# Performance work log

Measured on AMD Instinct MI355X. Metric: run time of the kernel, lower is better.

The kernel has to match this reference:

```python
import jax, jax.numpy as jnp
import numpy as np

N = 100_000   # nodes
E = 800_000   # edges
F_IN = 128    # num_features
E_IN = 64     # edge_dim
H = 100       # n_hidden
L = 2         # num_gnn_layers
BN_EPS = 1e-5


def _lin(key, fan_in, fan_out, extra=()):
    kw, _ = jax.random.split(key)
    w = jax.random.normal(kw, (*extra, fan_in, fan_out), jnp.float32) / np.float32(np.sqrt(fan_in))
    b = jnp.zeros((*extra, fan_out), jnp.float32)
    return w, b


def setup_inputs() -> dict:
    key = jax.random.key(0)
    ks = jax.random.split(key, 12)
    x = jax.random.normal(ks[0], (N, F_IN), jnp.float32)
    edge_index = jax.random.randint(ks[1], (2, E), 0, N, dtype=jnp.int32)
    edge_attr = jax.random.normal(ks[2], (E, E_IN), jnp.float32)
    node_w, node_b = _lin(ks[3], F_IN, H)
    edge_w, edge_b = _lin(ks[4], E_IN, H)
    lin_w, lin_b = _lin(ks[5], H, H, (L,))   # GINEConv edge lin per layer
    w1, b1 = _lin(ks[6], H, H, (L,))         # GINEConv nn first Linear
    w2, b2 = _lin(ks[7], H, H, (L,))         # GINEConv nn second Linear
    gamma = jnp.ones((L, H), jnp.float32)
    beta = jnp.zeros((L, H), jnp.float32)
    ew1, eb1 = _lin(ks[8], 3 * H, H, (L,))   # edge-update MLP
    ew2, eb2 = _lin(ks[9], H, H, (L,))
    mw1, mb1 = _lin(ks[10], 3 * H, 50)
    k11, k12 = jax.random.split(ks[11])
    mw2, mb2 = _lin(k11, 50, 25)
    mw3, mb3 = _lin(k12, 25, 2)
    return dict(x=x, edge_index=edge_index, edge_attr=edge_attr,
                node_w=node_w, node_b=node_b, edge_w=edge_w, edge_b=edge_b,
                lin_w=lin_w, lin_b=lin_b, w1=w1, b1=b1, w2=w2, b2=b2,
                gamma=gamma, beta=beta, ew1=ew1, eb1=eb1, ew2=ew2, eb2=eb2,
                mw1=mw1, mb1=mb1, mw2=mw2, mb2=mb2, mw3=mw3, mb3=mb3)


def reference(x, edge_index, edge_attr, node_w, node_b, edge_w, edge_b,
              lin_w, lin_b, w1, b1, w2, b2, gamma, beta,
              ew1, eb1, ew2, eb2, mw1, mb1, mw2, mb2, mw3, mb3):
    src, dst = edge_index[0], edge_index[1]
    h = x @ node_w + node_b          # [N, H]
    e = edge_attr @ edge_w + edge_b  # [E, H]
    for i in range(L):
        # GINEConv: message = relu(x_src + lin(edge_attr)); sum-aggregate at dst
        msg = jax.nn.relu(h[src] + (e @ lin_w[i] + lin_b[i]))       # [E, H]
        agg = jax.ops.segment_sum(msg, dst, num_segments=N)         # [N, H]
        z = h + agg                                                  # (1+eps)*x + aggr, eps=0
        z = jax.nn.relu(z @ w1[i] + b1[i]) @ w2[i] + b2[i]
        # BatchNorm over nodes (training mode, biased variance)
        mu = z.mean(0)
        var = z.var(0)
        z = (z - mu) * jax.lax.rsqrt(var + BN_EPS) * gamma[i] + beta[i]
        h = (h + jax.nn.relu(z)) / 2
        # edge update: emlp(cat(x_src, x_dst, e))
        cat = jnp.concatenate([h[src], h[dst], e], axis=-1)         # [E, 3H]
        e = e + (jax.nn.relu(cat @ ew1[i] + eb1[i]) @ ew2[i] + eb2[i]) / 2
    feat = jnp.concatenate(
        [jax.nn.relu(jnp.concatenate([h[src], h[dst]], axis=-1)), e], axis=1)  # [E, 3H]
    out = jax.nn.relu(feat @ mw1 + mb1)
    out = jax.nn.relu(out @ mw2 + mb2)
    return out @ mw3 + mb3  # [E, 2]
```

## Files before the change

### kernel.cpp

```cpp
#include <hip/hip_runtime.h>

#define N_NODES 100000
#define N_EDGES 800000
#define HDIM 100
#define LDP 112
#define TSTR 104

typedef __attribute__((ext_vector_type(8))) short bf16x8;
typedef __attribute__((ext_vector_type(4))) float f32x4;

__device__ inline uint packsplit(float v) {
    uint u = __float_as_uint(v);
    float r = v - __uint_as_float(u & 0xFFFF0000u);
    return (u & 0xFFFF0000u) | (__float_as_uint(r) >> 16);
}
__device__ inline float recw(uint w) {
    return __uint_as_float(w & 0xFFFF0000u) + __uint_as_float(w << 16);
}
__device__ inline uint4 relu4(uint4 a) {
    a.x &= ~(uint)((int)a.x >> 31); a.y &= ~(uint)((int)a.y >> 31);
    a.z &= ~(uint)((int)a.z >> 31); a.w &= ~(uint)((int)a.w >> 31);
    return a;
}
__device__ inline void unpack16(uint4 a, uint4 b, bf16x8& h8, bf16x8& l8) {
    union { uint u[4]; bf16x8 v; } H, L;
    H.u[0] = __builtin_amdgcn_perm(a.y, a.x, 0x07060302u);
    H.u[1] = __builtin_amdgcn_perm(a.w, a.z, 0x07060302u);
    H.u[2] = __builtin_amdgcn_perm(b.y, b.x, 0x07060302u);
    H.u[3] = __builtin_amdgcn_perm(b.w, b.z, 0x07060302u);
    L.u[0] = __builtin_amdgcn_perm(a.y, a.x, 0x05040100u);
    L.u[1] = __builtin_amdgcn_perm(a.w, a.z, 0x05040100u);
    L.u[2] = __builtin_amdgcn_perm(b.y, b.x, 0x05040100u);
    L.u[3] = __builtin_amdgcn_perm(b.w, b.z, 0x05040100u);
    h8 = H.v; l8 = L.v;
}
__device__ inline void split8(float4 a, float4 b, bf16x8& h8, bf16x8& l8) {
    float v[8] = {a.x, a.y, a.z, a.w, b.x, b.y, b.z, b.w};
    bf16x8 hh, ll;
#pragma unroll
    for (int i = 0; i < 8; ++i) {
        uint u = __float_as_uint(v[i]);
        hh[i] = (short)(u >> 16);
        float r = v[i] - __uint_as_float(u & 0xFFFF0000u);
        ll[i] = (short)(__float_as_uint(r) >> 16);
    }
    h8 = hh; l8 = ll;
}

template<int CONCAT>
__global__ __launch_bounds__(256)
void pack_k(const float* __restrict__ W, ushort* __restrict__ hi, ushort* __restrict__ lo,
            int K, int NC, int Kpad, int NCpad, int total)
{
    int idx = blockIdx.x * 256 + threadIdx.x;
    if (idx >= total) return;
    int per = NCpad * Kpad;
    int b = idx / per, rem = idx - b * per;
    int col = rem / Kpad, kv = rem - col * Kpad;
    int srck; bool valid;
    if (CONCAT) {
        int seg = kv >> 7, off = kv & 127;
        srck = seg * 100 + off;
        valid = (off < 100) && (srck < K) && (col < NC);
    } else {
        srck = kv;
        valid = (kv < K) && (col < NC);
    }
    float v = valid ? W[(long)b * K * NC + (long)srck * NC + col] : 0.f;
    uint w = packsplit(v);
    hi[idx] = (ushort)(w >> 16);
    lo[idx] = (ushort)(w & 0xFFFFu);
}

template<int TILES, int TPW, int STEPS, int MODE, int GATHER, int AFP32, int OUTF32, int CLAMP>
__global__ __launch_bounds__(256, 2)
void gemm9_k(const uint* aP, int lda, const float* __restrict__ aF, int ldaf,
             const ushort* __restrict__ wH, const ushort* __restrict__ wL,
             const float* __restrict__ bias,
             float* __restrict__ Cf, uint* cP, int ldc,
             int M, int NC, const int* __restrict__ g0)
{
    constexpr int KPADW = STEPS * 32;
    const int tid  = threadIdx.x;
    const int lane = tid & 63;
    const int w    = tid >> 6;
    const int cl   = lane & 15;
    const int kgrp = lane >> 4;
    const long row0 = (long)blockIdx.x * 64;

    int arows[4];
#pragma unroll
    for (int rg = 0; rg < 4; ++rg) {
        long grow = row0 + rg * 16 + cl;
        int gc = (int)((grow < M) ? grow : (M - 1));
        arows[rg] = (GATHER == 3) ? g0[gc] : gc;
    }

    uint4  aw0[2][4], aw1[2][4];
    float4 af0[2][4], af1[2][4];
    bf16x8 bh[2][TPW], bl[2][TPW];
    f32x4  acc[TPW][4];
#pragma unroll
    for (int tp = 0; tp < TPW; ++tp)
#pragma unroll
        for (int rg = 0; rg < 4; ++rg) acc[tp][rg] = (f32x4){0.f, 0.f, 0.f, 0.f};

    auto loadA = [&](int st, int sl) {
        const int kk = st * 32 + kgrp * 8;
#pragma unroll
        for (int rg = 0; rg < 4; ++rg) {
            if (AFP32) {
                const float* p = aF + (size_t)arows[rg] * ldaf + kk;
                af0[sl][rg] = *(const float4*)p;
                af1[sl][rg] = *(const float4*)(p + 4);
            } else {
                bool ok = !CLAMP || ((st & 3) != 3) || (kgrp == 0);
                if (ok) {
                    const uint* p = aP + (size_t)arows[rg] * lda + kk;
                    aw0[sl][rg] = *(const uint4*)p;
                    aw1[sl][rg] = *(const uint4*)(p + 4);
                } else {
                    aw0[sl][rg] = make_uint4(0, 0, 0, 0);
                    aw1[sl][rg] = make_uint4(0, 0, 0, 0);
                }
            }
        }
    };
    auto loadB = [&](int st, int sl) {
        int kk = st * 32 + kgrp * 8;
#pragma unroll
        for (int tp = 0; tp < TPW; ++tp) {
            int colw = (w * TPW + tp) * 16 + cl;
            bh[sl][tp] = *(const bf16x8*)(wH + (size_t)colw * KPADW + kk);
            bl[sl][tp] = *(const bf16x8*)(wL + (size_t)colw * KPADW + kk);
        }
    };

    loadA(0, 0); loadB(0, 0);
    if (STEPS > 1) { loadA(1, 1); loadB(1, 1); }

#pragma unroll
    for (int st = 0; st < STEPS; ++st) {
        const int sl = st & 1;
#pragma unroll
        for (int rg = 0; rg < 4; ++rg) {
            bf16x8 aH, aL;
            if (AFP32) split8(af0[sl][rg], af1[sl][rg], aH, aL);
            else       unpack16(aw0[sl][rg], aw1[sl][rg], aH, aL);
#pragma unroll
            for (int tp = 0; tp < TPW; ++tp) {
                acc[tp][rg] = __builtin_amdgcn_mfma_f32_16x16x32_bf16(aL, bh[sl][tp], acc[tp][rg], 0, 0, 0);
                acc[tp][rg] = __builtin_amdgcn_mfma_f32_16x16x32_bf16(aH, bl[sl][tp], acc[tp][rg], 0, 0, 0);
                acc[tp][rg] = __builtin_amdgcn_mfma_f32_16x16x32_bf16(aH, bh[sl][tp], acc[tp][rg], 0, 0, 0);
            }
        }
        if (st + 2 < STEPS) { loadA(st + 2, sl); loadB(st + 2, sl); }
    }

#pragma unroll
    for (int tp = 0; tp < TPW; ++tp) {
        int col = (w * TPW + tp) * 16 + cl;
        if (col >= NC) continue;
        float bv = bias[col];
#pragma unroll
        for (int rg = 0; rg < 4; ++rg) {
#pragma unroll
            for (int i = 0; i < 4; ++i) {
                long grow = row0 + rg * 16 + kgrp * 4 + i;
                if (grow >= M) continue;
                float v = acc[tp][rg][i] + bv;
                if (MODE == 1) v = fmaxf(v, 0.f);
                long o = grow * (long)ldc + col;
                if (OUTF32) Cf[o] = v;
                else        cP[o] = packsplit(v);
            }
        }
    }
}

__global__ __launch_bounds__(256, 2)
void fused_edge_k(const uint* __restrict__ hP, uint* eP,
                  const ushort* __restrict__ w1H, const ushort* __restrict__ w1L,
                  const float* __restrict__ b1v,
                  const ushort* __restrict__ w2H, const ushort* __restrict__ w2L,
                  const float* __restrict__ b2v,
                  const int* __restrict__ g0, const int* __restrict__ g1)
{
    __shared__ uint sm[64 * 128];
    const int tid = threadIdx.x, lane = tid & 63, w = tid >> 6;
    const int cl = lane & 15, kgrp = lane >> 4;
    const long row0 = (long)blockIdx.x * 64;

    int rs[4], rd[4];
#pragma unroll
    for (int rg = 0; rg < 4; ++rg) {
        long gr = row0 + rg * 16 + cl;
        rs[rg] = g0[gr]; rd[rg] = g1[gr];
    }

    uint4 aw0[2][4], aw1[2][4];
    bf16x8 bh[2][2], bl[2][2];
    f32x4 acc[2][4];
#pragma unroll
    for (int tp = 0; tp < 2; ++tp)
#pragma unroll
        for (int rg = 0; rg < 4; ++rg) acc[tp][rg] = (f32x4){0.f, 0.f, 0.f, 0.f};

    auto loadA = [&](int st, int sl) {
        int seg = st >> 2, inseg = (st & 3) * 32 + kgrp * 8;
        bool ok = ((st & 3) != 3) || (kgrp == 0);
        const uint* base = (seg == 2) ? eP : hP;
#pragma unroll
        for (int rg = 0; rg < 4; ++rg) {
            if (ok) {
                long row = (seg == 0) ? rs[rg] : (seg == 1) ? rd[rg] : (row0 + rg * 16 + cl);
                const uint* p = base + (size_t)row * LDP + inseg;
                aw0[sl][rg] = *(const uint4*)p;
                aw1[sl][rg] = *(const uint4*)(p + 4);
            } else {
                aw0[sl][rg] = make_uint4(0, 0, 0, 0);
                aw1[sl][rg] = make_uint4(0, 0, 0, 0);
            }
        }
    };
    auto loadB = [&](int st, int sl) {
        int kk = st * 32 + kgrp * 8;
#pragma unroll
        for (int tp = 0; tp < 2; ++tp) {
            int colw = (w * 2 + tp) * 16 + cl;
            bh[sl][tp] = *(const bf16x8*)(w1H + (size_t)colw * 384 + kk);
            bl[sl][tp] = *(const bf16x8*)(w1L + (size_t)colw * 384 + kk);
        }
    };

    loadA(0, 0); loadB(0, 0); loadA(1, 1); loadB(1, 1);
#pragma unroll
    for (int st = 0; st < 12; ++st) {
        const int sl = st & 1;
#pragma unroll
        for (int rg = 0; rg < 4; ++rg) {
            bf16x8 aH, aL;
            unpack16(aw0[sl][rg], aw1[sl][rg], aH, aL);
#pragma unroll
            for (int tp = 0; tp < 2; ++tp) {
                acc[tp][rg] = __builtin_amdgcn_mfma_f32_16x16x32_bf16(aL, bh[sl][tp], acc[tp][rg], 0, 0, 0);
                acc[tp][rg] = __builtin_amdgcn_mfma_f32_16x16x32_bf16(aH, bl[sl][tp], acc[tp][rg], 0, 0, 0);
                acc[tp][rg] = __builtin_amdgcn_mfma_f32_16x16x32_bf16(aH, bh[sl][tp], acc[tp][rg], 0, 0, 0);
            }
        }
        if (st + 2 < 12) { loadA(st + 2, sl); loadB(st + 2, sl); }
    }

#pragma unroll
    for (int tp = 0; tp < 2; ++tp) {
        int col = (w * 2 + tp) * 16 + cl;
        float bv = (col < 100) ? b1v[col] : 0.f;
#pragma unroll
        for (int rg = 0; rg < 4; ++rg)
#pragma unroll
            for (int i = 0; i < 4; ++i) {
                int row = rg * 16 + kgrp * 4 + i;
                uint u = 0;
                if (col < 100) u = packsplit(fmaxf(acc[tp][rg][i] + bv, 0.f));
                sm[row * 128 + (col ^ ((row & 7) << 2))] = u;
            }
    }
    __syncthreads();

    f32x4 acc2[2][4];
#pragma unroll
    for (int tp = 0; tp < 2; ++tp)
#pragma unroll
        for (int rg = 0; rg < 4; ++rg) acc2[tp][rg] = (f32x4){0.f, 0.f, 0.f, 0.f};
    bf16x8 ch[2][2], clo[2][2];
    auto loadB2 = [&](int st, int sl) {
        int kk = st * 32 + kgrp * 8;
#pragma unroll
        for (int tp = 0; tp < 2; ++tp) {
            int colw = (w * 2 + tp) * 16 + cl;
            ch[sl][tp]  = *(const bf16x8*)(w2H + (size_t)colw * 128 + kk);
            clo[sl][tp] = *(const bf16x8*)(w2L + (size_t)colw * 128 + kk);
        }
    };
    loadB2(0, 0); loadB2(1, 1);
#pragma unroll
    for (int st = 0; st < 4; ++st) {
        const int sl = st & 1;
#pragma unroll
        for (int rg = 0; rg < 4; ++rg) {
            int row = rg * 16 + cl;
            int swz = (row & 7) << 2, s4 = swz & 4;
            int k = st * 32 + kgrp * 8;
            int base = row * 128 + (k ^ (swz & 24));
            uint4 q0 = *(const uint4*)&sm[base + s4];
            uint4 q1 = *(const uint4*)&sm[base + (s4 ^ 4)];
            bf16x8 aH, aL;
            unpack16(q0, q1, aH, aL);
#pragma unroll
            for (int tp = 0; tp < 2; ++tp) {
                acc2[tp][rg] = __builtin_amdgcn_mfma_f32_16x16x32_bf16(aL, ch[sl][tp], acc2[tp][rg], 0, 0, 0);
                acc2[tp][rg] = __builtin_amdgcn_mfma_f32_16x16x32_bf16(aH, clo[sl][tp], acc2[tp][rg], 0, 0, 0);
                acc2[tp][rg] = __builtin_amdgcn_mfma_f32_16x16x32_bf16(aH, ch[sl][tp], acc2[tp][rg], 0, 0, 0);
            }
        }
        if (st + 2 < 4) loadB2(st + 2, sl);
    }
#pragma unroll
    for (int tp = 0; tp < 2; ++tp) {
        int col = (w * 2 + tp) * 16 + cl;
        if (col >= 100) continue;
        float bv = b2v[col];
#pragma unroll
        for (int rg = 0; rg < 4; ++rg)
#pragma unroll
            for (int i = 0; i < 4; ++i) {
                long grow = row0 + rg * 16 + kgrp * 4 + i;
                long o = grow * (long)LDP + col;
                float v = recw(eP[o]) + 0.5f * (acc2[tp][rg][i] + bv);
                eP[o] = packsplit(v);
            }
    }
}

__global__ __launch_bounds__(256, 2)
void fused_final_k(const uint* __restrict__ hP, const uint* __restrict__ eP,
                   const ushort* __restrict__ m1H, const ushort* __restrict__ m1L,
                   const float* __restrict__ mb1,
                   const ushort* __restrict__ m2H, const ushort* __restrict__ m2L,
                   const float* __restrict__ mb2, const float* __restrict__ mw3,
                   const float* __restrict__ mb3,
                   const int* __restrict__ g0, const int* __restrict__ g1,
                   const int* __restrict__ eidx, float* __restrict__ out)
{
    __shared__ uint sm[64 * 64];
    const int tid = threadIdx.x, lane = tid & 63, w = tid >> 6;
    const int cl = lane & 15, kgrp = lane >> 4;
    const long row0 = (long)blockIdx.x * 64;

    int rs[4], rd[4];
#pragma unroll
    for (int rg = 0; rg < 4; ++rg) {
        long gr = row0 + rg * 16 + cl;
        rs[rg] = g0[gr]; rd[rg] = g1[gr];
    }

    uint4 aw0[2][4], aw1[2][4];
    bf16x8 bh[2], bl[2];
    f32x4 acc1[4];
#pragma unroll
    for (int rg = 0; rg < 4; ++rg) acc1[rg] = (f32x4){0.f, 0.f, 0.f, 0.f};

    auto loadA = [&](int st, int sl) {
        int seg = st >> 2, inseg = (st & 3) * 32 + kgrp * 8;
        bool ok = ((st & 3) != 3) || (kgrp == 0);
        const uint* base = (seg == 2) ? eP : hP;
#pragma unroll
        for (int rg = 0; rg < 4; ++rg) {
            if (ok) {
                long row = (seg == 0) ? rs[rg] : (seg == 1) ? rd[rg] : (row0 + rg * 16 + cl);
                const uint* p = base + (size_t)row * LDP + inseg;
                aw0[sl][rg] = *(const uint4*)p;
                aw1[sl][rg] = *(const uint4*)(p + 4);
            } else {
                aw0[sl][rg] = make_uint4(0, 0, 0, 0);
                aw1[sl][rg] = make_uint4(0, 0, 0, 0);
            }
        }
    };
    auto loadB = [&](int st, int sl) {
        int kk = st * 32 + kgrp * 8;
        int colw = w * 16 + cl;
        bh[sl] = *(const bf16x8*)(m1H + (size_t)colw * 384 + kk);
        bl[sl] = *(const bf16x8*)(m1L + (size_t)colw * 384 + kk);
    };

    loadA(0, 0); loadB(0, 0); loadA(1, 1); loadB(1, 1);
#pragma unroll
    for (int st = 0; st < 12; ++st) {
        const int sl = st & 1;
#pragma unroll
        for (int rg = 0; rg < 4; ++rg) {
            uint4 w0 = aw0[sl][rg], w1 = aw1[sl][rg];
            if (st < 8) { w0 = relu4(w0); w1 = relu4(w1); }
            bf16x8 aH, aL;
            unpack16(w0, w1, aH, aL);
            acc1[rg] = __builtin_amdgcn_mfma_f32_16x16x32_bf16(aL, bh[sl], acc1[rg], 0, 0, 0);
            acc1[rg] = __builtin_amdgcn_mfma_f32_16x16x32_bf16(aH, bl[sl], acc1[rg], 0, 0, 0);
            acc1[rg] = __builtin_amdgcn_mfma_f32_16x16x32_bf16(aH, bh[sl], acc1[rg], 0, 0, 0);
        }
        if (st + 2 < 12) { loadA(st + 2, sl); loadB(st + 2, sl); }
    }

    {
        int col = w * 16 + cl;
        float bv = (col < 50) ? mb1[col] : 0.f;
#pragma unroll
        for (int rg = 0; rg < 4; ++rg)
#pragma unroll
            for (int i = 0; i < 4; ++i) {
                int row = rg * 16 + kgrp * 4 + i;
                uint u = 0;
                if (col < 50) u = packsplit(fmaxf(acc1[rg][i] + bv, 0.f));
                sm[row * 64 + (col ^ ((row & 7) << 2))] = u;
            }
    }
    __syncthreads();

    bf16x8 c2h[2][2], c2l[2][2];
#pragma unroll
    for (int t = 0; t < 2; ++t)
#pragma unroll
        for (int st = 0; st < 2; ++st) {
            long o = (long)(t * 16 + cl) * 64 + st * 32 + kgrp * 8;
            c2h[t][st] = *(const bf16x8*)(m2H + o);
            c2l[t][st] = *(const bf16x8*)(m2L + o);
        }
    const float bias0 = mb2[cl];
    const float bias1 = (cl + 16 < 25) ? mb2[cl + 16] : 0.f;
    const float w3a0 = mw3[cl * 2 + 0], w3a1 = mw3[cl * 2 + 1];
    const float w3b0 = (cl + 16 < 25) ? mw3[(cl + 16) * 2 + 0] : 0.f;
    const float w3b1 = (cl + 16 < 25) ? mw3[(cl + 16) * 2 + 1] : 0.f;
    const float b30 = mb3[0], b31 = mb3[1];

    const int row = w * 16 + cl;
    const int swz = (row & 7) << 2, s4 = swz & 4;
    f32x4 a0 = (f32x4){0.f, 0.f, 0.f, 0.f}, a1 = a0;
#pragma unroll
    for (int st = 0; st < 2; ++st) {
        int k = st * 32 + kgrp * 8;
        int base = row * 64 + (k ^ (swz & 24));
        uint4 q0 = *(const uint4*)&sm[base + s4];
        uint4 q1 = *(const uint4*)&sm[base + (s4 ^ 4)];
        bf16x8 aH, aL;
        unpack16(q0, q1, aH, aL);
        a0 = __builtin_amdgcn_mfma_f32_16x16x32_bf16(aL, c2h[0][st], a0, 0, 0, 0);
        a0 = __builtin_amdgcn_mfma_f32_16x16x32_bf16(aH, c2l[0][st], a0, 0, 0, 0);
        a0 = __builtin_amdgcn_mfma_f32_16x16x32_bf16(aH, c2h[0][st], a0, 0, 0, 0);
        a1 = __builtin_amdgcn_mfma_f32_16x16x32_bf16(aL, c2h[1][st], a1, 0, 0, 0);
        a1 = __builtin_amdgcn_mfma_f32_16x16x32_bf16(aH, c2l[1][st], a1, 0, 0, 0);
        a1 = __builtin_amdgcn_mfma_f32_16x16x32_bf16(aH, c2h[1][st], a1, 0, 0, 0);
    }
#pragma unroll
    for (int i = 0; i < 4; ++i) {
        float t0 = fmaxf(a0[i] + bias0, 0.f);
        float t1 = fmaxf(a1[i] + bias1, 0.f);
        float s0 = t0 * w3a0 + t1 * w3b0;
        float s1 = t0 * w3a1 + t1 * w3b1;
#pragma unroll
        for (int d = 1; d < 16; d <<= 1) {
            s0 += __shfl_xor(s0, d, 64);
            s1 += __shfl_xor(s1, d, 64);
        }
        if (cl == 0) {
            long grow = row0 + w * 16 + kgrp * 4 + i;
            int oe = eidx[grow];
            out[(long)oe * 2 + 0] = s0 + b30;
            out[(long)oe * 2 + 1] = s1 + b31;
        }
    }
}

__global__ __launch_bounds__(256)
void hist_k(const int* __restrict__ dst, int* __restrict__ cnt)
{
    int e = blockIdx.x * 256 + threadIdx.x;
    if (e < N_EDGES) atomicAdd(&cnt[dst[e]], 1);
}

__global__ __launch_bounds__(1024)
void scan_k(const int* __restrict__ cnt, int* __restrict__ off)
{
    __shared__ int part[1024];
    const int t = threadIdx.x;
    const int per = (N_NODES + 1023) / 1024;
    const int base = t * per;
    int s = 0;
    for (int i = 0; i < per; ++i) {
        int n = base + i;
        if (n < N_NODES) s += cnt[n];
    }
    part[t] = s;
    __syncthreads();
    for (int d = 1; d < 1024; d <<= 1) {
        int v = (t >= d) ? part[t - d] : 0;
        __syncthreads();
        part[t] += v;
        __syncthreads();
    }
    int run = (t == 0) ? 0 : part[t - 1];
    for (int i = 0; i < per; ++i) {
        int n = base + i;
        if (n < N_NODES) { off[n] = run; run += cnt[n]; }
    }
    if (t == 1023) off[N_NODES] = run;
}

__global__ __launch_bounds__(256)
void fill_k(const int* __restrict__ dst, const int* __restrict__ off,
            int* __restrict__ pos, int* __restrict__ eidx)
{
    int e = blockIdx.x * 256 + threadIdx.x;
    if (e >= N_EDGES) return;
    int d = dst[e];
    int p = atomicAdd(&pos[d], 1);
    eidx[off[d] + p] = e;
}

__global__ __launch_bounds__(256)
void perm_k(const int* __restrict__ eidx, const int* __restrict__ src,
            const int* __restrict__ dst, int* __restrict__ psrc, int* __restrict__ pdst)
{
    int j = blockIdx.x * 256 + threadIdx.x;
    if (j >= N_EDGES) return;
    int e = eidx[j];
    psrc[j] = src[e];
    pdst[j] = dst[e];
}

__global__ __launch_bounds__(256)
void agg_k(const uint* __restrict__ hP, const float* __restrict__ tmp,
           const int* __restrict__ psrc, const int* __restrict__ off,
           uint* __restrict__ aP)
{
    unsigned idx = blockIdx.x * 256u + threadIdx.x;
    if (idx >= (unsigned)(N_NODES * 26)) return;
    unsigned n = idx / 26u;
    unsigned q = (idx - n * 26u) * 4u;
    long ob = (long)n * LDP + q;
    if (q >= 100) {
        *(uint4*)&aP[ob] = make_uint4(0, 0, 0, 0);
        return;
    }
    uint4 hw = *(const uint4*)&hP[ob];
    float a0 = recw(hw.x), a1 = recw(hw.y), a2 = recw(hw.z), a3 = recw(hw.w);
    int j0 = off[n], j1 = off[n + 1];
    for (int j = j0; j < j1; ++j) {
        long sb = (long)psrc[j] * LDP + q;
        uint4 sw = *(const uint4*)&hP[sb];
        float4 t = *(const float4*)&tmp[(long)j * TSTR + q];
        a0 += fmaxf(recw(sw.x) + t.x, 0.f);
        a1 += fmaxf(recw(sw.y) + t.y, 0.f);
        a2 += fmaxf(recw(sw.z) + t.z, 0.f);
        a3 += fmaxf(recw(sw.w) + t.w, 0.f);
    }
    *(uint4*)&aP[ob] = make_uint4(packsplit(a0), packsplit(a1), packsplit(a2), packsplit(a3));
}

__global__ __launch_bounds__(128)
void bn_stats_k(const float* __restrict__ z, float* __restrict__ stats)
{
    int c = threadIdx.x;
    if (c >= HDIM) return;
    long rows_per = (N_NODES + gridDim.x - 1) / gridDim.x;
    long r0 = (long)blockIdx.x * rows_per;
    long r1 = r0 + rows_per; if (r1 > N_NODES) r1 = N_NODES;
    float s = 0.f, s2 = 0.f;
    for (long r = r0; r < r1; ++r) {
        float v = z[r * TSTR + c];
        s += v; s2 += v * v;
    }
    atomicAdd(&stats[c], s);
    atomicAdd(&stats[HDIM + c], s2);
}

__global__ __launch_bounds__(256)
void bn_apply_k(const float* __restrict__ z2, const float* __restrict__ stats,
                const float* __restrict__ gamma, const float* __restrict__ beta,
                uint* __restrict__ hP)
{
    unsigned idx = blockIdx.x * 256u + threadIdx.x;
    if (idx >= (unsigned)(N_NODES * 25)) return;
    unsigned n = idx / 25u;
    unsigned q = (idx - n * 25u) * 4u;
    const float invN = 1.f / N_NODES;
    long ob = (long)n * LDP + q;
    uint4 hw = *(const uint4*)&hP[ob];
    float4 zv = *(const float4*)&z2[(long)n * TSTR + q];
    float hv[4] = {recw(hw.x), recw(hw.y), recw(hw.z), recw(hw.w)};
    float zz[4] = {zv.x, zv.y, zv.z, zv.w};
    float r[4];
#pragma unroll
    for (int i = 0; i < 4; ++i) {
        unsigned c = q + i;
        float mu  = stats[c] * invN;
        float var = stats[HDIM + c] * invN - mu * mu;
        float v = (zz[i] - mu) * rsqrtf(var + 1e-5f) * gamma[c] + beta[c];
        r[i] = (hv[i] + fmaxf(v, 0.f)) * 0.5f;
    }
    *(uint4*)&hP[ob] = make_uint4(packsplit(r[0]), packsplit(r[1]), packsplit(r[2]), packsplit(r[3]));
}

static inline int gb64(long m) { return (int)((m + 63) / 64); }

extern "C" void kernel_launch(void* const* d_in, const int* in_sizes, int n_in,
                              void* d_out, int out_size, void* d_ws, size_t ws_size,
                              hipStream_t stream)
{
    const float* x         = (const float*)d_in[0];
    const int*   ei        = (const int*)  d_in[1];
    const float* edge_attr = (const float*)d_in[2];
    const float* node_w    = (const float*)d_in[3];
    const float* node_b    = (const float*)d_in[4];
    const float* edge_w    = (const float*)d_in[5];
    const float* edge_b    = (const float*)d_in[6];
    const float* lin_w     = (const float*)d_in[7];
    const float* lin_b     = (const float*)d_in[8];
    const float* w1        = (const float*)d_in[9];
    const float* b1        = (const float*)d_in[10];
    const float* w2        = (const float*)d_in[11];
    const float* b2        = (const float*)d_in[12];
    const float* gamma     = (const float*)d_in[13];
    const float* beta      = (const float*)d_in[14];
    const float* ew1       = (const float*)d_in[15];
    const float* eb1       = (const float*)d_in[16];
    const float* ew2       = (const float*)d_in[17];
    const float* eb2       = (const float*)d_in[18];
    const float* mw1       = (const float*)d_in[19];
    const float* mb1       = (const float*)d_in[20];
    const float* mw2       = (const float*)d_in[21];
    const float* mb2       = (const float*)d_in[22];
    const float* mw3       = (const float*)d_in[23];
    const float* mb3       = (const float*)d_in[24];
    float* out = (float*)d_out;

    ushort* pw = (ushort*)d_ws;
    size_t off_w = 0;
    ushort *nwH, *nwL, *ewH, *ewL, *liH, *liL, *w1H, *w1L, *w2H, *w2L,
           *e1H, *e1L, *e2H, *e2L, *m1H, *m1L, *m2H, *m2L;
    auto nextw = [&](size_t s, ushort*& H, ushort*& L) { H = pw + off_w; L = pw + off_w + s; off_w += 2 * s; };
    nextw(128 * 128,     nwH, nwL);
    nextw(128 * 64,      ewH, ewL);
    nextw(2 * 128 * 128, liH, liL);
    nextw(2 * 128 * 128, w1H, w1L);
    nextw(2 * 128 * 128, w2H, w2L);
    nextw(2 * 128 * 384, e1H, e1L);
    nextw(2 * 128 * 128, e2H, e2L);
    nextw(64 * 384,      m1H, m1L);
    nextw(32 * 64,       m2H, m2L);

    int* intb = (int*)((char*)d_ws + (2u << 20));
    int* cnt   = intb;
    int* coff  = cnt + N_NODES;
    int* pos   = coff + N_NODES + 1;
    int* eidx  = pos + N_NODES;
    int* psrc  = eidx + N_EDGES;
    int* pdst  = psrc + N_EDGES;
    float* stats = (float*)(pdst + N_EDGES);

    char* fbase = (char*)d_ws + (16u << 20);
    uint* eP = (uint*)fbase;
    uint* hP = eP + (size_t)N_EDGES * LDP;
    uint* aP = hP + (size_t)N_NODES * LDP;
    char* big = (char*)(aP + (size_t)N_NODES * LDP);
    float* tmp = (float*)big;
    float* z2  = (float*)big;

    const int* srcp = ei;
    const int* dstp = ei + N_EDGES;
    dim3 blk(256);

    auto packl = [&](const float* W, ushort* H, ushort* L, int K, int NC, int Kp, int NCp, int batch, bool cc) {
        int total = batch * NCp * Kp;
        if (cc) pack_k<1><<<(total + 255) / 256, blk, 0, stream>>>(W, H, L, K, NC, Kp, NCp, total);
        else    pack_k<0><<<(total + 255) / 256, blk, 0, stream>>>(W, H, L, K, NC, Kp, NCp, total);
    };
    packl(node_w, nwH, nwL, 128, 100, 128, 128, 1, false);
    packl(edge_w, ewH, ewL,  64, 100,  64, 128, 1, false);
    packl(lin_w,  liH, liL, 100, 100, 128, 128, 2, false);
    packl(w1,     w1H, w1L, 100, 100, 128, 128, 2, false);
    packl(w2,     w2H, w2L, 100, 100, 128, 128, 2, false);
    packl(ew1,    e1H, e1L, 300, 100, 384, 128, 2, true);
    packl(ew2,    e2H, e2L, 100, 100, 128, 128, 2, false);
    packl(mw1,    m1H, m1L, 300,  50, 384,  64, 1, true);
    packl(mw2,    m2H, m2L,  50,  25,  64,  32, 1, false);

    hipMemsetAsync(cnt, 0, N_NODES * sizeof(int), stream);
    hist_k<<<(N_EDGES + 255) / 256, blk, 0, stream>>>(dstp, cnt);
    scan_k<<<1, dim3(1024), 0, stream>>>(cnt, coff);
    hipMemsetAsync(pos, 0, N_NODES * sizeof(int), stream);
    fill_k<<<(N_EDGES + 255) / 256, blk, 0, stream>>>(dstp, coff, pos, eidx);
    perm_k<<<(N_EDGES + 255) / 256, blk, 0, stream>>>(eidx, srcp, dstp, psrc, pdst);

    gemm9_k<8,2,4,0,0,1,0,0><<<gb64(N_NODES), blk, 0, stream>>>(
        nullptr, 0, x, 128, nwH, nwL, node_b, nullptr, hP, LDP, N_NODES, 100, nullptr);
    gemm9_k<8,2,2,0,3,1,0,0><<<gb64(N_EDGES), blk, 0, stream>>>(
        nullptr, 0, edge_attr, 64, ewH, ewL, edge_b, nullptr, eP, LDP, N_EDGES, 100, eidx);

    for (int i = 0; i < 2; ++i) {
        gemm9_k<8,2,4,0,0,0,1,1><<<gb64(N_EDGES), blk, 0, stream>>>(
            eP, LDP, nullptr, 0, liH + (size_t)i * 16384, liL + (size_t)i * 16384,
            lin_b + i * HDIM, tmp, nullptr, TSTR, N_EDGES, 100, nullptr);
        agg_k<<<(N_NODES * 26 + 255) / 256, blk, 0, stream>>>(hP, tmp, psrc, coff, aP);
        gemm9_k<8,2,4,1,0,0,0,1><<<gb64(N_NODES), blk, 0, stream>>>(
            aP, LDP, nullptr, 0, w1H + (size_t)i * 16384, w1L + (size_t)i * 16384,
            b1 + i * HDIM, nullptr, aP, LDP, N_NODES, 100, nullptr);
        gemm9_k<8,2,4,0,0,0,1,1><<<gb64(N_NODES), blk, 0, stream>>>(
            aP, LDP, nullptr, 0, w2H + (size_t)i * 16384, w2L + (size_t)i * 16384,
            b2 + i * HDIM, z2, nullptr, TSTR, N_NODES, 100, nullptr);
        hipMemsetAsync(stats, 0, 2 * HDIM * sizeof(float), stream);
        bn_stats_k<<<1024, dim3(128), 0, stream>>>(z2, stats);
        bn_apply_k<<<(N_NODES * 25 + 255) / 256, blk, 0, stream>>>(
            z2, stats, gamma + i * HDIM, beta + i * HDIM, hP);
        fused_edge_k<<<gb64(N_EDGES), blk, 0, stream>>>(
            hP, eP,
            e1H + (size_t)i * 49152, e1L + (size_t)i * 49152, eb1 + i * HDIM,
            e2H + (size_t)i * 16384, e2L + (size_t)i * 16384, eb2 + i * HDIM,
            psrc, pdst);
    }

    fused_final_k<<<gb64(N_EDGES), blk, 0, stream>>>(
        hP, eP, m1H, m1L, mb1, m2H, m2L, mb2, mw3, mb3, psrc, pdst, eidx, out);
}
```

Measured before the change: 3.860 ms.

## Fuse edge-lin GEMM with message relu and dst-sorted segment aggregation

```diff
diff --git a/kernel.cpp b/kernel.cpp
--- a/kernel.cpp
+++ b/kernel.cpp
@@ -179,6 +179,119 @@
 }
 
 __global__ __launch_bounds__(256, 2)
+void msg_agg_k(const uint* __restrict__ eP,
+               const ushort* __restrict__ wH, const ushort* __restrict__ wL,
+               const float* __restrict__ bias,
+               const uint* __restrict__ hP,
+               const int* __restrict__ psrc, const int* __restrict__ pdst,
+               float* __restrict__ aggF)
+{
+    __shared__ float sm[64 * 108];
+    __shared__ int sd[64];
+    const int tid = threadIdx.x, lane = tid & 63, w = tid >> 6;
+    const int cl = lane & 15, kgrp = lane >> 4;
+    const long row0 = (long)blockIdx.x * 64;
+
+    if (tid < 64) sd[tid] = pdst[row0 + tid];
+
+    int sr[4][4];
+#pragma unroll
+    for (int rg = 0; rg < 4; ++rg)
+#pragma unroll
+        for (int i = 0; i < 4; ++i)
+            sr[rg][i] = psrc[row0 + rg * 16 + kgrp * 4 + i];
+
+    uint4 aw0[2][4], aw1[2][4];
+    bf16x8 bh[2][2], bl[2][2];
+    f32x4 acc[2][4];
+#pragma unroll
+    for (int tp = 0; tp < 2; ++tp)
+#pragma unroll
+        for (int rg = 0; rg < 4; ++rg) acc[tp][rg] = (f32x4){0.f, 0.f, 0.f, 0.f};
+
+    auto loadA = [&](int st, int sl) {
+        const int kk = st * 32 + kgrp * 8;
+        bool ok = ((st & 3) != 3) || (kgrp == 0);
+#pragma unroll
+        for (int rg = 0; rg < 4; ++rg) {
+            if (ok) {
+                const uint* p = eP + (size_t)(row0 + rg * 16 + cl) * LDP + kk;
+                aw0[sl][rg] = *(const uint4*)p;
+                aw1[sl][rg] = *(const uint4*)(p + 4);
+            } else {
+                aw0[sl][rg] = make_uint4(0, 0, 0, 0);
+                aw1[sl][rg] = make_uint4(0, 0, 0, 0);
+            }
+        }
+    };
+    auto loadB = [&](int st, int sl) {
+        int kk = st * 32 + kgrp * 8;
+#pragma unroll
+        for (int tp = 0; tp < 2; ++tp) {
+            int colw = (w * 2 + tp) * 16 + cl;
+            bh[sl][tp] = *(const bf16x8*)(wH + (size_t)colw * 128 + kk);
+            bl[sl][tp] = *(const bf16x8*)(wL + (size_t)colw * 128 + kk);
+        }
+    };
+
+    loadA(0, 0); loadB(0, 0); loadA(1, 1); loadB(1, 1);
+#pragma unroll
+    for (int st = 0; st < 4; ++st) {
+        const int sl = st & 1;
+#pragma unroll
+        for (int rg = 0; rg < 4; ++rg) {
+            bf16x8 aH, aL;
+            unpack16(aw0[sl][rg], aw1[sl][rg], aH, aL);
+#pragma unroll
+            for (int tp = 0; tp < 2; ++tp) {
+                acc[tp][rg] = __builtin_amdgcn_mfma_f32_16x16x32_bf16(aL, bh[sl][tp], acc[tp][rg], 0, 0, 0);
+                acc[tp][rg] = __builtin_amdgcn_mfma_f32_16x16x32_bf16(aH, bl[sl][tp], acc[tp][rg], 0, 0, 0);
+                acc[tp][rg] = __builtin_amdgcn_mfma_f32_16x16x32_bf16(aH, bh[sl][tp], acc[tp][rg], 0, 0, 0);
+            }
+        }
+        if (st + 2 < 4) { loadA(st + 2, sl); loadB(st + 2, sl); }
+    }
+
+#pragma unroll
+    for (int tp = 0; tp < 2; ++tp) {
+        int col = (w * 2 + tp) * 16 + cl;
+        if (col < 100) {
+            float bv = bias[col];
+#pragma unroll
+            for (int rg = 0; rg < 4; ++rg)
+#pragma unroll
+                for (int i = 0; i < 4; ++i) {
+                    int row = rg * 16 + kgrp * 4 + i;
+                    float hv = recw(hP[(size_t)sr[rg][i] * LDP + col]);
+                    sm[row * 108 + col] = fmaxf(acc[tp][rg][i] + bv + hv, 0.f);
+                }
+        }
+    }
+    __syncthreads();
+
+    if (tid < 100) {
+        const int c = tid;
+        int cur = sd[0];
+        float s = 0.f;
+        bool first = true;
+        for (int r = 0; r < 64; ++r) {
+            int d = sd[r];
+            if (d != cur) {
+                bool contPrev = first && (row0 > 0) && (pdst[row0 - 1] == cur);
+                if (contPrev) atomicAdd(&aggF[(size_t)cur * TSTR + c], s);
+                else aggF[(size_t)cur * TSTR + c] = recw(hP[(size_t)cur * LDP + c]) + s;
+                first = false; s = 0.f; cur = d;
+            }
+            s += sm[r * 108 + c];
+        }
+        bool contPrev = first && (row0 > 0) && (pdst[row0 - 1] == cur);
+        bool contNext = (row0 + 64 < N_EDGES) && (pdst[row0 + 64] == cur);
+        if (contPrev || contNext) atomicAdd(&aggF[(size_t)cur * TSTR + c], s);
+        else aggF[(size_t)cur * TSTR + c] = recw(hP[(size_t)cur * LDP + c]) + s;
+    }
+}
+
+__global__ __launch_bounds__(256, 2)
 void fused_edge_k(const uint* __restrict__ hP, uint* eP,
                   const ushort* __restrict__ w1H, const ushort* __restrict__ w1L,
                   const float* __restrict__ b1v,
@@ -186,7 +299,7 @@
                   const float* __restrict__ b2v,
                   const int* __restrict__ g0, const int* __restrict__ g1)
 {
-    __shared__ uint sm[64 * 128];
+    __shared__ uint sm[64 * 108];
     const int tid = threadIdx.x, lane = tid & 63, w = tid >> 6;
     const int cl = lane & 15, kgrp = lane >> 4;
     const long row0 = (long)blockIdx.x * 64;
@@ -254,16 +367,18 @@
 #pragma unroll
     for (int tp = 0; tp < 2; ++tp) {
         int col = (w * 2 + tp) * 16 + cl;
-        float bv = (col < 100) ? b1v[col] : 0.f;
-#pragma unroll
-        for (int rg = 0; rg < 4; ++rg)
-#pragma unroll
-            for (int i = 0; i < 4; ++i) {
-                int row = rg * 16 + kgrp * 4 + i;
-                uint u = 0;
-                if (col < 100) u = packsplit(fmaxf(acc[tp][rg][i] + bv, 0.f));
-                sm[row * 128 + (col ^ ((row & 7) << 2))] = u;
-            }
+        if (col < 108) {
+            float bv = (col < 100) ? b1v[col] : 0.f;
+#pragma unroll
+            for (int rg = 0; rg < 4; ++rg)
+#pragma unroll
+                for (int i = 0; i < 4; ++i) {
+                    int row = rg * 16 + kgrp * 4 + i;
+                    uint u = 0;
+                    if (col < 100) u = packsplit(fmaxf(acc[tp][rg][i] + bv, 0.f));
+                    sm[row * 108 + col] = u;
+                }
+        }
     }
     __syncthreads();
 
@@ -289,11 +404,12 @@
 #pragma unroll
         for (int rg = 0; rg < 4; ++rg) {
             int row = rg * 16 + cl;
-            int swz = (row & 7) << 2, s4 = swz & 4;
-            int k = st * 32 + kgrp * 8;
-            int base = row * 128 + (k ^ (swz & 24));
-            uint4 q0 = *(const uint4*)&sm[base + s4];
-            uint4 q1 = *(const uint4*)&sm[base + (s4 ^ 4)];
+            int kk = st * 32 + kgrp * 8;
+            uint4 q0 = make_uint4(0, 0, 0, 0), q1 = make_uint4(0, 0, 0, 0);
+            if ((st != 3) || (kgrp == 0)) {
+                q0 = *(const uint4*)&sm[row * 108 + kk];
+                q1 = *(const uint4*)&sm[row * 108 + kk + 4];
+            }
             bf16x8 aH, aL;
             unpack16(q0, q1, aH, aL);
 #pragma unroll
@@ -332,7 +448,7 @@
                    const int* __restrict__ g0, const int* __restrict__ g1,
                    const int* __restrict__ eidx, float* __restrict__ out)
 {
-    __shared__ uint sm[64 * 64];
+    __shared__ uint sm[64 * 68];
     const int tid = threadIdx.x, lane = tid & 63, w = tid >> 6;
     const int cl = lane & 15, kgrp = lane >> 4;
     const long row0 = (long)blockIdx.x * 64;
@@ -401,7 +517,7 @@
                 int row = rg * 16 + kgrp * 4 + i;
                 uint u = 0;
                 if (col < 50) u = packsplit(fmaxf(acc1[rg][i] + bv, 0.f));
-                sm[row * 64 + (col ^ ((row & 7) << 2))] = u;
+                sm[row * 68 + col] = u;
             }
     }
     __syncthreads();
@@ -423,14 +539,12 @@
     const float b30 = mb3[0], b31 = mb3[1];
 
     const int row = w * 16 + cl;
-    const int swz = (row & 7) << 2, s4 = swz & 4;
     f32x4 a0 = (f32x4){0.f, 0.f, 0.f, 0.f}, a1 = a0;
 #pragma unroll
     for (int st = 0; st < 2; ++st) {
-        int k = st * 32 + kgrp * 8;
-        int base = row * 64 + (k ^ (swz & 24));
-        uint4 q0 = *(const uint4*)&sm[base + s4];
-        uint4 q1 = *(const uint4*)&sm[base + (s4 ^ 4)];
+        int kk = st * 32 + kgrp * 8;
+        uint4 q0 = *(const uint4*)&sm[row * 68 + kk];
+        uint4 q1 = *(const uint4*)&sm[row * 68 + kk + 4];
         bf16x8 aH, aL;
         unpack16(q0, q1, aH, aL);
         a0 = __builtin_amdgcn_mfma_f32_16x16x32_bf16(aL, c2h[0][st], a0, 0, 0, 0);
@@ -518,32 +632,19 @@
 }
 
 __global__ __launch_bounds__(256)
-void agg_k(const uint* __restrict__ hP, const float* __restrict__ tmp,
-           const int* __restrict__ psrc, const int* __restrict__ off,
-           uint* __restrict__ aP)
+void h2agg_k(const uint* __restrict__ hP, float* __restrict__ aggF)
 {
     unsigned idx = blockIdx.x * 256u + threadIdx.x;
     if (idx >= (unsigned)(N_NODES * 26)) return;
     unsigned n = idx / 26u;
     unsigned q = (idx - n * 26u) * 4u;
-    long ob = (long)n * LDP + q;
+    long ob = (long)n * TSTR + q;
     if (q >= 100) {
-        *(uint4*)&aP[ob] = make_uint4(0, 0, 0, 0);
+        *(float4*)&aggF[ob] = make_float4(0.f, 0.f, 0.f, 0.f);
         return;
     }
-    uint4 hw = *(const uint4*)&hP[ob];
-    float a0 = recw(hw.x), a1 = recw(hw.y), a2 = recw(hw.z), a3 = recw(hw.w);
-    int j0 = off[n], j1 = off[n + 1];
-    for (int j = j0; j < j1; ++j) {
-        long sb = (long)psrc[j] * LDP + q;
-        uint4 sw = *(const uint4*)&hP[sb];
-        float4 t = *(const float4*)&tmp[(long)j * TSTR + q];
-        a0 += fmaxf(recw(sw.x) + t.x, 0.f);
-        a1 += fmaxf(recw(sw.y) + t.y, 0.f);
-        a2 += fmaxf(recw(sw.z) + t.z, 0.f);
-        a3 += fmaxf(recw(sw.w) + t.w, 0.f);
-    }
-    *(uint4*)&aP[ob] = make_uint4(packsplit(a0), packsplit(a1), packsplit(a2), packsplit(a3));
+    uint4 hw = *(const uint4*)&hP[(long)n * LDP + q];
+    *(float4*)&aggF[ob] = make_float4(recw(hw.x), recw(hw.y), recw(hw.z), recw(hw.w));
 }
 
 __global__ __launch_bounds__(128)
@@ -650,10 +751,10 @@
     char* fbase = (char*)d_ws + (16u << 20);
     uint* eP = (uint*)fbase;
     uint* hP = eP + (size_t)N_EDGES * LDP;
-    uint* aP = hP + (size_t)N_NODES * LDP;
-    char* big = (char*)(aP + (size_t)N_NODES * LDP);
-    float* tmp = (float*)big;
-    float* z2  = (float*)big;
+    uint* zP = hP + (size_t)N_NODES * LDP;
+    char* big = (char*)(zP + (size_t)N_NODES * LDP);
+    float* aggF = (float*)big;
+    float* z2   = aggF + (size_t)N_NODES * TSTR;
 
     const int* srcp = ei;
     const int* dstp = ei + N_EDGES;
@@ -687,15 +788,15 @@
         nullptr, 0, edge_attr, 64, ewH, ewL, edge_b, nullptr, eP, LDP, N_EDGES, 100, eidx);
 
     for (int i = 0; i < 2; ++i) {
-        gemm9_k<8,2,4,0,0,0,1,1><<<gb64(N_EDGES), blk, 0, stream>>>(
-            eP, LDP, nullptr, 0, liH + (size_t)i * 16384, liL + (size_t)i * 16384,
-            lin_b + i * HDIM, tmp, nullptr, TSTR, N_EDGES, 100, nullptr);
-        agg_k<<<(N_NODES * 26 + 255) / 256, blk, 0, stream>>>(hP, tmp, psrc, coff, aP);
-        gemm9_k<8,2,4,1,0,0,0,1><<<gb64(N_NODES), blk, 0, stream>>>(
-            aP, LDP, nullptr, 0, w1H + (size_t)i * 16384, w1L + (size_t)i * 16384,
-            b1 + i * HDIM, nullptr, aP, LDP, N_NODES, 100, nullptr);
+        h2agg_k<<<(N_NODES * 26 + 255) / 256, blk, 0, stream>>>(hP, aggF);
+        msg_agg_k<<<gb64(N_EDGES), blk, 0, stream>>>(
+            eP, liH + (size_t)i * 16384, liL + (size_t)i * 16384, lin_b + i * HDIM,
+            hP, psrc, pdst, aggF);
+        gemm9_k<8,2,4,1,0,1,0,0><<<gb64(N_NODES), blk, 0, stream>>>(
+            nullptr, 0, aggF, TSTR, w1H + (size_t)i * 16384, w1L + (size_t)i * 16384,
+            b1 + i * HDIM, nullptr, zP, LDP, N_NODES, 100, nullptr);
         gemm9_k<8,2,4,0,0,0,1,1><<<gb64(N_NODES), blk, 0, stream>>>(
-            aP, LDP, nullptr, 0, w2H + (size_t)i * 16384, w2L + (size_t)i * 16384,
+            zP, LDP, nullptr, 0, w2H + (size_t)i * 16384, w2L + (size_t)i * 16384,
             b2 + i * HDIM, z2, nullptr, TSTR, N_NODES, 100, nullptr);
         hipMemsetAsync(stats, 0, 2 * HDIM * sizeof(float), stream);
         bn_stats_k<<<1024, dim3(128), 0, stream>>>(z2, stats);
```

After: 3.550 ms. -8.0%, faster.
